# Performance work log

Hardware: AMD Instinct MI355X
Metric: run time of the kernel (lower is better)

Reference implementation:

```python
import jax, jax.numpy as jnp
import numpy as np

N, C_IN, C_OUT, K, S, P, H, W = 16, 64, 128, 3, 1, 1, 224, 224

def setup_inputs() -> dict:
    key = jax.random.key(0)
    kx, kw = jax.random.split(key)
    x = jax.random.normal(kx, (N, C_IN, H, W), dtype=jnp.float32)
    weight = jax.random.normal(kw, (C_OUT, C_IN, K, K), dtype=jnp.float32)
    bias = jnp.zeros((C_OUT,), dtype=jnp.float32)
    return {"x": x, "weight": weight, "bias": bias}

def reference(x, weight, bias):
    # im2col + matmul with stride 1 is exactly a standard conv2d with SAME-style padding P
    out = jax.lax.conv_general_dilated(
        x, weight,
        window_strides=(S, S),
        padding=((P, P), (P, P)),
        dimension_numbers=("NCHW", "OIHW", "NCHW"),
    )
    return out + bias[None, :, None, None]  # [N, C_OUT, H, W]
```

## Files before the change

### kernel.cpp

```cpp
#include <hip/hip_runtime.h>
#include <cstdint>
#include <cstddef>


typedef short bf16x8 __attribute__((ext_vector_type(8)));
typedef float f32x4 __attribute__((ext_vector_type(4)));

#define N_ 16
#define CI_ 64
#define CO_ 128
#define H_ 224
#define W_ 224
#define HW_ (H_ * W_)

#define WP_ 226
#define CBS_ 1808ULL
#define HPS_ 14464ULL
#define NS_ 3268864ULL

#define ROWBUF_SHORTS 7296
#define CONV3_LDS 145408

__device__ __forceinline__ unsigned short f2bf(float f) {
    unsigned u = __builtin_bit_cast(unsigned, f);
    u += 0x7FFFu + ((u >> 16) & 1u);
    return (unsigned short)(u >> 16);
}

__global__ void prep_weight(const float* __restrict__ w, unsigned short* __restrict__ wr) {
    int i = blockIdx.x * 256 + threadIdx.x;
    if (i >= 9 * CO_ * CI_) return;
    int ci = i & 63;
    int co = (i >> 6) & 127;
    int t  = i >> 13;
    wr[i] = f2bf(w[(co * CI_ + ci) * 9 + t]);
}

__global__ __launch_bounds__(256) void prep_x(const float* __restrict__ x,
                                              unsigned short* __restrict__ xp) {
    int b = blockIdx.x;
    int n = b / 226, hp = b - n * 226;
    int tid = threadIdx.x;
    unsigned short* row = xp + (size_t)n * NS_ + (size_t)hp * HPS_;
    if (hp == 0 || hp == 225) {
        #pragma unroll
        for (int k = 0; k < 8; ++k) {
            int i = k * 256 + tid;
            if (i < 1808) ((uint4*)row)[i] = make_uint4(0, 0, 0, 0);
        }
        return;
    }
    int h = hp - 1;
    const float* xb = x + (size_t)n * CI_ * HW_ + (size_t)h * W_;
    for (int k = 0; k < 7; ++k) {
        int item = k * 256 + tid;
        int w = item % 224;
        int cb = item / 224;
        unsigned r[4];
        #pragma unroll
        for (int c = 0; c < 4; ++c) {
            float lo = xb[(size_t)(cb * 8 + 2 * c) * HW_ + w];
            float hi = xb[(size_t)(cb * 8 + 2 * c + 1) * HW_ + w];
            r[c] = (unsigned)f2bf(lo) | ((unsigned)f2bf(hi) << 16);
        }
        *(uint4*)(row + (size_t)cb * CBS_ + (size_t)(w + 1) * 8) = make_uint4(r[0], r[1], r[2], r[3]);
    }
    if (tid < 16) {
        int cb = tid >> 1, wp = (tid & 1) * 225;
        *(uint4*)(row + (size_t)cb * CBS_ + (size_t)wp * 8) = make_uint4(0, 0, 0, 0);
    }
}

__global__ __launch_bounds__(512, 2) void conv3(
    const unsigned short* __restrict__ xp, const unsigned short* __restrict__ wr,
    const float* __restrict__ bias, float* __restrict__ out)
{
    extern __shared__ __align__(16) unsigned short ring[];
    float* bounce = (float*)ring + 6 * ROWBUF_SHORTS / 2;

    int bid = blockIdx.x;
    int swz = (bid & 7) * 32 + (bid >> 3);
    int n = swz >> 4;
    int rem = swz & 15;
    int wseg = rem & 1;
    int strip = rem >> 1;
    int ho0 = strip * 28;

    int tid = threadIdx.x, lane = tid & 63, wid = tid >> 6;
    int hr = wid & 1, mq = wid >> 1;
    int lrow = lane & 15, lk = lane >> 4;

    const unsigned short* xpn = xp + (size_t)n * NS_;

    auto stage_row = [&](int hp) {
        const unsigned short* srow = xpn + (size_t)hp * HPS_ + (size_t)(wseg * 112) * 8;
        unsigned short* dbase = ring + (size_t)(hp % 6) * ROWBUF_SHORTS;
        int idx = tid;
        {
            int cb = idx / 114, wp = idx - cb * 114;
            __builtin_amdgcn_global_load_lds(
                (const __attribute__((address_space(1))) void*)(srow + (size_t)cb * CBS_ + (size_t)wp * 8),
                (__attribute__((address_space(3))) void*)(dbase + (size_t)idx * 8), 16, 0, 0);
        }
        idx = 512 + tid;
        if (idx < 912) {
            int cb = idx / 114, wp = idx - cb * 114;
            __builtin_amdgcn_global_load_lds(
                (const __attribute__((address_space(1))) void*)(srow + (size_t)cb * CBS_ + (size_t)wp * 8),
                (__attribute__((address_space(3))) void*)(dbase + (size_t)idx * 8), 16, 0, 0);
        }
    };

    stage_row(ho0); stage_row(ho0 + 1); stage_row(ho0 + 2); stage_row(ho0 + 3);
    __syncthreads();

    #pragma unroll 1
    for (int i = 0; i < 14; ++i) {
        int ho = ho0 + 2 * i;

        if (i < 13) { stage_row(ho + 4); stage_row(ho + 5); }

        f32x4 acc[2][7];
        #pragma unroll
        for (int a = 0; a < 2; ++a)
            #pragma unroll
            for (int b2 = 0; b2 < 7; ++b2)
                #pragma unroll
                for (int k = 0; k < 4; ++k)
                    acc[a][b2][k] = 0.0f;

        #pragma unroll
        for (int ch = 0; ch < 2; ++ch) {
            #pragma unroll
            for (int t = 0; t < 9; ++t) {
                int kh = t / 3, kw = t - kh * 3;
                bf16x8 afr[2];
                #pragma unroll
                for (int mf = 0; mf < 2; ++mf) {
                    size_t ai = ((size_t)(t * 128 + mq * 32 + mf * 16 + lrow)) * 64
                              + (size_t)(ch * 32 + lk * 8);
                    afr[mf] = *(const bf16x8*)(wr + ai);
                }
                int slot = (ho + hr + kh) % 6;
                int rb = slot * ROWBUF_SHORTS + ((ch * 4 + lk) * 114) * 8;
                int wb = lrow + kw;
                #pragma unroll
                for (int nf = 0; nf < 7; ++nf) {
                    bf16x8 bfr = *(const bf16x8*)(ring + rb + (size_t)(wb + nf * 16) * 8);
                    acc[0][nf] = __builtin_amdgcn_mfma_f32_16x16x32_bf16(afr[0], bfr, acc[0][nf], 0, 0, 0);
                    acc[1][nf] = __builtin_amdgcn_mfma_f32_16x16x32_bf16(afr[1], bfr, acc[1][nf], 0, 0, 0);
                }
            }
        }

        float* lf = bounce + wid * 1808;
        int h = ho + hr;
        #pragma unroll
        for (int mf = 0; mf < 2; ++mf) {
            float bv[4];
            #pragma unroll
            for (int r = 0; r < 4; ++r)
                bv[r] = bias[mq * 32 + mf * 16 + lk * 4 + r];
            float* wbase = lf + lk * 452 + lrow;
            #pragma unroll
            for (int r = 0; r < 4; ++r)
                #pragma unroll
                for (int nf = 0; nf < 7; ++nf)
                    wbase[r * 112 + nf * 16] = acc[mf][nf][r] + bv[r];
            #pragma unroll
            for (int j = 0; j < 7; ++j) {
                int idx4 = j * 64 + lane;
                int col = idx4 / 28;
                int w4  = idx4 - col * 28;
                f32x4 v = *(const f32x4*)(lf + (col >> 2) * 452 + (col & 3) * 112 + w4 * 4);
                size_t ob = (((size_t)n * CO_ + mq * 32 + mf * 16 + col) * H_ + h) * W_
                          + wseg * 112 + w4 * 4;
                *(f32x4*)(out + ob) = v;
            }
        }

        __builtin_amdgcn_sched_barrier(0);
        asm volatile("s_waitcnt vmcnt(14) lgkmcnt(0)" ::: "memory");
        __builtin_amdgcn_s_barrier();
        __builtin_amdgcn_sched_barrier(0);
    }
}

__global__ __launch_bounds__(256, 2) void conv2(
    const unsigned short* __restrict__ xp, const unsigned short* __restrict__ wr,
    const float* __restrict__ bias, float* __restrict__ out)
{
    __shared__ __align__(16) unsigned short xs[4 * 8 * 114 * 8];

    int bid = blockIdx.x;
    int swz = (bid & 7) * 448 + (bid >> 3);
    int n = swz / 224;
    int r2 = swz - n * 224;
    int hblk = r2 >> 1;
    int wseg = r2 & 1;
    int h0 = hblk * 2;

    int tid = threadIdx.x, lane = tid & 63, wid = tid >> 6;
    int hr = wid & 1, mh = wid >> 1;
    int lrow = lane & 15, lk = lane >> 4;

    f32x4 acc[4][7];
    #pragma unroll
    for (int a = 0; a < 4; ++a)
        #pragma unroll
        for (int b2 = 0; b2 < 7; ++b2)
            #pragma unroll
            for (int k = 0; k < 4; ++k)
                acc[a][b2][k] = 0.0f;

    const unsigned short* xpn = xp + (size_t)n * NS_;

    #pragma unroll
    for (int it = 0; it < 14; ++it) {
        int idx = it * 256 + tid;
        int wp = idx % 114;
        int rc = idx / 114;
        const unsigned short* src = xpn + (size_t)(h0 + (rc >> 3)) * HPS_
                                  + (size_t)(rc & 7) * CBS_ + (size_t)(wseg * 112 + wp) * 8;
        __builtin_amdgcn_global_load_lds(
            (const __attribute__((address_space(1))) void*)src,
            (__attribute__((address_space(3))) void*)(xs + (size_t)idx * 8), 16, 0, 0);
    }
    if (tid < 64) {
        int idx = 3584 + tid;
        int wp = idx % 114;
        int rc = idx / 114;
        const unsigned short* src = xpn + (size_t)(h0 + (rc >> 3)) * HPS_
                                  + (size_t)(rc & 7) * CBS_ + (size_t)(wseg * 112 + wp) * 8;
        __builtin_amdgcn_global_load_lds(
            (const __attribute__((address_space(1))) void*)src,
            (__attribute__((address_space(3))) void*)(xs + (size_t)idx * 8), 16, 0, 0);
    }
    __syncthreads();

    #pragma unroll
    for (int ch = 0; ch < 2; ++ch) {
        #pragma unroll
        for (int t = 0; t < 9; ++t) {
            int kh = t / 3, kw = t - kh * 3;
            bf16x8 afr[4];
            #pragma unroll
            for (int mf = 0; mf < 4; ++mf) {
                size_t ai = ((size_t)(t * 128 + mh * 64 + mf * 16 + lrow)) * 64
                          + (size_t)(ch * 32 + lk * 8);
                afr[mf] = *(const bf16x8*)(wr + ai);
            }
            int rbase = ((hr + kh) * 8 + ch * 4 + lk) * 114;
            int wpb = lrow + kw;
            #pragma unroll
            for (int nf = 0; nf < 7; ++nf) {
                bf16x8 bfr = *(const bf16x8*)(&xs[(size_t)(rbase + wpb + nf * 16) * 8]);
                #pragma unroll
                for (int mf = 0; mf < 4; ++mf)
                    acc[mf][nf] = __builtin_amdgcn_mfma_f32_16x16x32_bf16(
                        afr[mf], bfr, acc[mf][nf], 0, 0, 0);
            }
        }
    }

    __syncthreads();
    float* lf = (float*)xs;
    int h = h0 + hr;
    #pragma unroll
    for (int mf = 0; mf < 4; ++mf) {
        float bv[4];
        #pragma unroll
        for (int r = 0; r < 4; ++r)
            bv[r] = bias[mh * 64 + mf * 16 + lk * 4 + r];
        float* wbase = lf + wid * 1808 + lk * 452 + lrow;
        #pragma unroll
        for (int r = 0; r < 4; ++r)
            #pragma unroll
            for (int nf = 0; nf < 7; ++nf)
                wbase[r * 112 + nf * 16] = acc[mf][nf][r] + bv[r];
        #pragma unroll
        for (int j = 0; j < 7; ++j) {
            int idx4 = j * 64 + lane;
            int col = idx4 / 28;
            int w4  = idx4 - col * 28;
            f32x4 v = *(const f32x4*)(lf + wid * 1808 + (col >> 2) * 452 + (col & 3) * 112 + w4 * 4);
            size_t ob = (((size_t)n * CO_ + mh * 64 + mf * 16 + col) * H_ + h) * W_
                      + wseg * 112 + w4 * 4;
            *(f32x4*)(out + ob) = v;
        }
    }
}

extern "C" void kernel_launch(void* const* d_in, const int* in_sizes, int n_in,
                              void* d_out, int out_size, void* d_ws, size_t ws_size,
                              hipStream_t stream) {
    const float* x    = (const float*)d_in[0];
    const float* w    = (const float*)d_in[1];
    const float* bias = (const float*)d_in[2];
    float* out = (float*)d_out;
    unsigned short* wr = (unsigned short*)d_ws;
    const size_t xp_bytes = (size_t)N_ * NS_ * 2;
    const size_t need = 147456 + xp_bytes;

    prep_weight<<<dim3(288), dim3(256), 0, stream>>>(w, wr);
    if (ws_size >= need) {
        unsigned short* xp = wr + 73728;
        prep_x<<<dim3(16 * 226), dim3(256), 0, stream>>>(x, xp);
        hipError_t e = hipFuncSetAttribute(
            reinterpret_cast<const void*>(conv3),
            hipFuncAttributeMaxDynamicSharedMemorySize, CONV3_LDS);
        if (e == hipSuccess) {
            conv3<<<dim3(256), dim3(512), CONV3_LDS, stream>>>(xp, wr, bias, out);
        } else {
            conv2<<<dim3(16 * 112 * 2), dim3(256), 0, stream>>>(xp, wr, bias, out);
        }
    }
}
```

Measured before the change: 244.4 us.

## Retile conv3 warps to 64 channels by 64/48 columns for fragment reuse

```diff
diff --git a/kernel.cpp b/kernel.cpp
--- a/kernel.cpp
+++ b/kernel.cpp
@@ -5,6 +5,8 @@
 
 typedef short bf16x8 __attribute__((ext_vector_type(8)));
 typedef float f32x4 __attribute__((ext_vector_type(4)));
+
+template<int V> struct IC { static constexpr int value = V; };
 
 #define N_ 16
 #define CI_ 64
@@ -85,15 +87,23 @@
     int wseg = rem & 1;
     int strip = rem >> 1;
     int ho0 = strip * 28;
+    int w0 = wseg * 112;
 
     int tid = threadIdx.x, lane = tid & 63, wid = tid >> 6;
-    int hr = wid & 1, mq = wid >> 1;
+    int hr = wid & 1, mh = (wid >> 1) & 1, nh = wid >> 2;
     int lrow = lane & 15, lk = lane >> 4;
 
     const unsigned short* xpn = xp + (size_t)n * NS_;
 
+    float bv[4][4];
+    #pragma unroll
+    for (int mf = 0; mf < 4; ++mf)
+        #pragma unroll
+        for (int r = 0; r < 4; ++r)
+            bv[mf][r] = bias[mh * 64 + mf * 16 + lk * 4 + r];
+
     auto stage_row = [&](int hp) {
-        const unsigned short* srow = xpn + (size_t)hp * HPS_ + (size_t)(wseg * 112) * 8;
+        const unsigned short* srow = xpn + (size_t)hp * HPS_ + (size_t)w0 * 8;
         unsigned short* dbase = ring + (size_t)(hp % 6) * ROWBUF_SHORTS;
         int idx = tid;
         {
@@ -120,67 +130,70 @@
 
         if (i < 13) { stage_row(ho + 4); stage_row(ho + 5); }
 
-        f32x4 acc[2][7];
-        #pragma unroll
-        for (int a = 0; a < 2; ++a)
-            #pragma unroll
-            for (int b2 = 0; b2 < 7; ++b2)
-                #pragma unroll
-                for (int k = 0; k < 4; ++k)
-                    acc[a][b2][k] = 0.0f;
-
-        #pragma unroll
-        for (int ch = 0; ch < 2; ++ch) {
-            #pragma unroll
-            for (int t = 0; t < 9; ++t) {
-                int kh = t / 3, kw = t - kh * 3;
-                bf16x8 afr[2];
-                #pragma unroll
-                for (int mf = 0; mf < 2; ++mf) {
-                    size_t ai = ((size_t)(t * 128 + mq * 32 + mf * 16 + lrow)) * 64
-                              + (size_t)(ch * 32 + lk * 8);
-                    afr[mf] = *(const bf16x8*)(wr + ai);
-                }
-                int slot = (ho + hr + kh) % 6;
-                int rb = slot * ROWBUF_SHORTS + ((ch * 4 + lk) * 114) * 8;
-                int wb = lrow + kw;
-                #pragma unroll
-                for (int nf = 0; nf < 7; ++nf) {
-                    bf16x8 bfr = *(const bf16x8*)(ring + rb + (size_t)(wb + nf * 16) * 8);
-                    acc[0][nf] = __builtin_amdgcn_mfma_f32_16x16x32_bf16(afr[0], bfr, acc[0][nf], 0, 0, 0);
-                    acc[1][nf] = __builtin_amdgcn_mfma_f32_16x16x32_bf16(afr[1], bfr, acc[1][nf], 0, 0, 0);
+        auto body = [&](auto NFC_) {
+            constexpr int NFC = decltype(NFC_)::value;
+            f32x4 acc[4][NFC];
+            #pragma unroll
+            for (int a = 0; a < 4; ++a)
+                #pragma unroll
+                for (int b2 = 0; b2 < NFC; ++b2)
+                    #pragma unroll
+                    for (int k = 0; k < 4; ++k)
+                        acc[a][b2][k] = 0.0f;
+
+            #pragma unroll
+            for (int ch = 0; ch < 2; ++ch) {
+                #pragma unroll
+                for (int t = 0; t < 9; ++t) {
+                    int kh = t / 3, kw = t - kh * 3;
+                    bf16x8 afr[4];
+                    #pragma unroll
+                    for (int mf = 0; mf < 4; ++mf) {
+                        size_t ai = ((size_t)(t * 128 + mh * 64 + mf * 16 + lrow)) * 64
+                                  + (size_t)(ch * 32 + lk * 8);
+                        afr[mf] = *(const bf16x8*)(wr + ai);
+                    }
+                    int slot = (ho + hr + kh) % 6;
+                    int rb = slot * ROWBUF_SHORTS + ((ch * 4 + lk) * 114) * 8;
+                    int wpb = nh * 64 + lrow + kw;
+                    #pragma unroll
+                    for (int nf = 0; nf < NFC; ++nf) {
+                        bf16x8 bfr = *(const bf16x8*)(ring + rb + (size_t)(wpb + nf * 16) * 8);
+                        #pragma unroll
+                        for (int mf = 0; mf < 4; ++mf)
+                            acc[mf][nf] = __builtin_amdgcn_mfma_f32_16x16x32_bf16(
+                                afr[mf], bfr, acc[mf][nf], 0, 0, 0);
+                    }
                 }
             }
-        }
-
-        float* lf = bounce + wid * 1808;
-        int h = ho + hr;
-        #pragma unroll
-        for (int mf = 0; mf < 2; ++mf) {
-            float bv[4];
-            #pragma unroll
-            for (int r = 0; r < 4; ++r)
-                bv[r] = bias[mq * 32 + mf * 16 + lk * 4 + r];
-            float* wbase = lf + lk * 452 + lrow;
-            #pragma unroll
-            for (int r = 0; r < 4; ++r)
-                #pragma unroll
-                for (int nf = 0; nf < 7; ++nf)
-                    wbase[r * 112 + nf * 16] = acc[mf][nf][r] + bv[r];
-            #pragma unroll
-            for (int j = 0; j < 7; ++j) {
-                int idx4 = j * 64 + lane;
-                int col = idx4 / 28;
-                int w4  = idx4 - col * 28;
-                f32x4 v = *(const f32x4*)(lf + (col >> 2) * 452 + (col & 3) * 112 + w4 * 4);
-                size_t ob = (((size_t)n * CO_ + mq * 32 + mf * 16 + col) * H_ + h) * W_
-                          + wseg * 112 + w4 * 4;
-                *(f32x4*)(out + ob) = v;
+
+            float* bw = bounce + wid * 1088;
+            int h = ho + hr;
+            constexpr int ROUNDS = (NFC == 4) ? 4 : 3;
+            constexpr int WQ     = (NFC == 4) ? 16 : 12;
+            #pragma unroll
+            for (int mf = 0; mf < 4; ++mf) {
+                #pragma unroll
+                for (int r = 0; r < 4; ++r)
+                    #pragma unroll
+                    for (int nf = 0; nf < NFC; ++nf)
+                        bw[(lk * 4 + r) * 68 + nf * 16 + lrow] = acc[mf][nf][r] + bv[mf][r];
+                #pragma unroll
+                for (int j = 0; j < ROUNDS; ++j) {
+                    int idx4 = j * 64 + lane;
+                    int c16 = idx4 / WQ;
+                    int w4  = idx4 - c16 * WQ;
+                    f32x4 v = *(const f32x4*)(bw + c16 * 68 + w4 * 4);
+                    size_t ob = (((size_t)n * CO_ + (mh * 64 + mf * 16 + c16)) * H_ + h) * W_
+                              + w0 + nh * 64 + w4 * 4;
+                    *(f32x4*)(out + ob) = v;
+                }
             }
-        }
+        };
+        if (nh == 0) body(IC<4>{}); else body(IC<3>{});
 
         __builtin_amdgcn_sched_barrier(0);
-        asm volatile("s_waitcnt vmcnt(14) lgkmcnt(0)" ::: "memory");
+        asm volatile("s_waitcnt vmcnt(12) lgkmcnt(0)" ::: "memory");
         __builtin_amdgcn_s_barrier();
         __builtin_amdgcn_sched_barrier(0);
     }
```

New measurement: 560.3 us. 2.29x slower.
